# Performance work log

Hardware: AMD Instinct MI355X
Metric: run time of the kernel (lower is better)

Reference implementation:

```python
import jax, jax.numpy as jnp
import numpy as np

B, S, H, K = 8, 2048, 768, 128
FILTERS = (1, 3, 5)
C = H // len(FILTERS)  # 256 channels per conv, concat -> H
LN_EPS = 1e-05
COS_EPS = 1e-08


def setup_inputs() -> dict:
    key = jax.random.key(0)
    ks = jax.random.split(key, 16)
    mk = lambda k, shape: jax.random.normal(k, shape, dtype=jnp.float32) * 0.02
    return {
        "representation": jax.random.normal(ks[0], (B, S, H), dtype=jnp.float32),
        "src_mask": jnp.ones((B, S), dtype=jnp.float32),
        # conv weights stored as [k, H_in, C_out] for lax 1D conv (torch Conv2d(1,C,(k,H)))
        "enc_conv_w1": mk(ks[1], (1, H, C)),
        "enc_conv_w3": mk(ks[2], (3, H, C)),
        "enc_conv_w5": mk(ks[3], (5, H, C)),
        "ln_g": jnp.ones((H,), jnp.float32),
        "ln_b": jnp.zeros((H,), jnp.float32),
        "enc_lin_w": mk(ks[4], (H, H)),   # torch Linear weight [out,in]
        "enc_tr_w": mk(ks[5], (K, H)),
        "dec_tr_w": mk(ks[6], (H, K)),
        "dec_conv_w1": mk(ks[7], (1, H, C)),
        "dec_conv_w3": mk(ks[8], (3, H, C)),
        "dec_conv_w5": mk(ks[9], (5, H, C)),
        "dec_lin_w": mk(ks[10], (H, H)),
        "out_lin_w": mk(ks[11], (H, H)),
    }


def _multi_conv(x, ws):
    # x: [B, S, H]; each w: [k, H, C]; torch pads (k//2, 0) -> same-length for odd k
    outs = []
    for w in ws:
        k = w.shape[0]
        outs.append(jax.lax.conv_general_dilated(
            x, w, window_strides=(1,), padding=[(k // 2, k // 2)],
            dimension_numbers=("NWC", "WIO", "NWC")))
    return jnp.concatenate(outs, axis=-1)  # [B, S, H]


def _layernorm(x, g, b):
    mu = jnp.mean(x, axis=-1, keepdims=True)
    var = jnp.mean((x - mu) ** 2, axis=-1, keepdims=True)
    return (x - mu) * jax.lax.rsqrt(var + LN_EPS) * g + b


def reference(representation, src_mask, enc_conv_w1, enc_conv_w3, enc_conv_w5,
              ln_g, ln_b, enc_lin_w, enc_tr_w, dec_tr_w,
              dec_conv_w1, dec_conv_w3, dec_conv_w5, dec_lin_w, out_lin_w):
    # ---- AutoEncoder (dropout layers are identity in eval mode) ----
    h = _multi_conv(representation, (enc_conv_w1, enc_conv_w3, enc_conv_w5))
    h = _layernorm(h + representation, ln_g, ln_b)
    h = jnp.tanh(h @ enc_lin_w.T)
    location = h @ enc_tr_w.T            # [B, S, K] (encode_out)
    d = location @ dec_tr_w.T            # [B, S, H]
    d = _multi_conv(d, (dec_conv_w1, dec_conv_w3, dec_conv_w5))
    d = jnp.tanh(d @ dec_lin_w.T)
    decode_out = d @ out_lin_w.T         # [B, S, H]

    # ---- banded pairwise cosine similarity (fuses the torch shift loop) ----
    # torch loop writes dis_matrix[b, i, i+s+1] = cos(loc[b, i+s+1], loc[b, i])
    # for s in range(max_act_len), i.e. the strict upper band of the symmetric
    # pairwise cosine-similarity matrix with offsets 1..max_act_len.
    normed = location / jnp.maximum(
        jnp.sqrt(jnp.sum(location * location, axis=-1, keepdims=True)), COS_EPS)
    sim = jnp.einsum("bid,bjd->bij", normed, normed)  # [B, S, S]
    offs = jnp.arange(S)[None, :] - jnp.arange(S)[:, None]  # j - i
    max_act_len = jnp.max(jnp.sum(src_mask, axis=-1)).astype(jnp.int32)
    band = (offs >= 1) & (offs <= max_act_len)        # [S, S]
    dis_matrix = jnp.where(band[None], sim, 0.0)
    src_dis_mask = src_mask[:, :, None] * src_mask[:, None, :]
    act_dis_tags = band[None].astype(jnp.float32) * src_dis_mask
    return (location, dis_matrix, act_dis_tags, decode_out)
```

## Files before the change

kernel.cpp:

```cpp
#include <hip/hip_runtime.h>

#define B_   8
#define S_   2048
#define H_   768
#define K_   128
#define C_   256
#define SH_  2052
#define MTOK (B_*S_)

typedef __attribute__((ext_vector_type(8))) short short8;
typedef __attribute__((ext_vector_type(4))) float f32x4;

typedef __attribute__((address_space(1))) const void gvoid;
typedef __attribute__((address_space(3))) void lvoid;

__device__ __forceinline__ void gload16(const void* g, void* l) {
    __builtin_amdgcn_global_load_lds((gvoid*)g, (lvoid*)l, 16, 0, 0);
}

__device__ __forceinline__ ushort f2b(float f) {
    union { float f; unsigned u; } v; v.f = f;
    unsigned r = v.u + 0x7fffu + ((v.u >> 16) & 1u);
    return (ushort)(r >> 16);
}
__device__ __forceinline__ float b2f(ushort u) {
    union { unsigned u; float f; } v; v.u = ((unsigned)u) << 16;
    return v.f;
}
__device__ __forceinline__ float fast_tanh(float x) {
    float e = __expf(2.f * x);
    return 1.f - 2.f / (e + 1.f);
}


__global__ __launch_bounds__(512) void k_maxlen(const float* __restrict__ mask, int* Lp,
                                                ushort* __restrict__ lh) {
    __shared__ float sh[8];
    const int tid = threadIdx.x;
    float mx = 0.f;
    for (int b = 0; b < B_; ++b) {
        const float4 v = ((const float4*)(mask + b * S_))[tid];
        float s = v.x + v.y + v.z + v.w;
#pragma unroll
        for (int off = 32; off; off >>= 1) s += __shfl_xor(s, off);
        if ((tid & 63) == 0) sh[tid >> 6] = s;
        __syncthreads();
        if (tid == 0) {
            float t = 0.f;
#pragma unroll
            for (int q = 0; q < 8; ++q) t += sh[q];
            mx = fmaxf(mx, t);
        }
        __syncthreads();
    }
    if (tid == 0) *Lp = (int)mx;
    for (int i = tid; i < B_ * 4 * K_; i += 512) {
        const int b = i >> 9;
        const int rc = i & 511;
        const int rr = rc >> 7;
        const int cc = rc & 127;
        const int row = (rr < 2) ? rr : (2048 + rr);
        lh[((size_t)b * SH_ + row) * K_ + cc] = 0;
    }
}

__global__ void k_build_xh(const float* __restrict__ rep, ushort* __restrict__ xh) {
    int i = blockIdx.x * blockDim.x + threadIdx.x;
    const int stride = gridDim.x * blockDim.x;
    const int n4 = B_ * SH_ * H_ / 4;
    for (; i < n4; i += stride) {
        const int idx = i * 4;
        const int h = idx % H_;
        const int rs = idx / H_;
        const int s = rs % SH_;
        const int b = rs / SH_;
        ushort4 o; o.x = 0; o.y = 0; o.z = 0; o.w = 0;
        if (s >= 2 && s < S_ + 2) {
            const float4 v = *(const float4*)(rep + ((size_t)b * S_ + (s - 2)) * H_ + h);
            o.x = f2b(v.x); o.y = f2b(v.y); o.z = f2b(v.z); o.w = f2b(v.w);
        }
        *(ushort4*)(xh + idx) = o;
    }
}

struct CvtE { const float* src; ushort* dst; int n; int kh; int sld; };
struct CvtAll { CvtE e[11]; };

__global__ void k_cvt_all(CvtAll a) {
    const CvtE e = a.e[blockIdx.y];
    int i = blockIdx.x * blockDim.x + threadIdx.x;
    const int stride = gridDim.x * blockDim.x;
    for (; i < e.n; i += stride) {
        if (e.kh) {
            const int c = i / e.kh;
            const int r = i - c * e.kh;
            e.dst[i] = f2b(e.src[r * e.sld + c]);
        } else {
            e.dst[i] = f2b(e.src[i]);
        }
    }
}


struct CompE { const ushort* w; int wld; int woff; ushort* o; int old_; int koff; };
struct CompP { const ushort* dtrT; CompE e[9]; };

__global__ __launch_bounds__(256) void k_compw(CompP p) {
    __shared__ __align__(16) ushort As[128 * 64];
    __shared__ __align__(16) ushort Bs[128 * 64];
    const CompE e = p.e[blockIdx.y];
    const int tid = threadIdx.x;
    const int w = tid >> 6, lane = tid & 63;
    const int l15 = lane & 15, lk = lane >> 4;
    const int wr = w >> 1, wc = w & 1;
    const int n_base = blockIdx.x * 128;
    f32x4 acc[4][4] = {};
    const int srow = lane >> 3;
    const int scol = (lane & 7) * 8;

    for (int kt = 0; kt < 12; ++kt) {
        const int kk = kt << 6;
#pragma unroll
        for (int q = 0; q < 4; ++q) {
            const int r = w * 32 + q * 8;
            gload16(p.dtrT + (size_t)(r + srow) * 768 + kk + scol, As + r * 64);
            gload16(e.w + (size_t)(n_base + r + srow) * e.wld + e.woff + kk + scol, Bs + r * 64);
        }
        __syncthreads();
#pragma unroll
        for (int ks = 0; ks < 2; ++ks) {
            short8 af[4], bfr[4];
#pragma unroll
            for (int i = 0; i < 4; ++i)
                af[i] = *(const short8*)(As + (wr * 64 + i * 16 + l15) * 64 + ks * 32 + 8 * lk);
#pragma unroll
            for (int j = 0; j < 4; ++j)
                bfr[j] = *(const short8*)(Bs + (wc * 64 + j * 16 + l15) * 64 + ks * 32 + 8 * lk);
#pragma unroll
            for (int i = 0; i < 4; ++i)
#pragma unroll
                for (int j = 0; j < 4; ++j)
                    acc[i][j] = __builtin_amdgcn_mfma_f32_16x16x32_bf16(af[i], bfr[j], acc[i][j], 0, 0, 0);
        }
        __syncthreads();
    }
#pragma unroll
    for (int i = 0; i < 4; ++i)
#pragma unroll
        for (int j = 0; j < 4; ++j)
#pragma unroll
            for (int jj = 0; jj < 4; ++jj) {
                const int jr = wr * 64 + i * 16 + 4 * lk + jj;
                const int c  = n_base + wc * 64 + j * 16 + l15;
                e.o[(size_t)c * e.old_ + e.koff + jr] = f2b(acc[i][j][jj]);
            }
}


struct G3P {
    const ushort* A;
    const ushort* W0;
    const ushort* W1;
    const ushort* W2;
    int lda;
    ushort* outB; int ldoB;
    int nMtiles;
};

template<bool DEC>
__global__ __launch_bounds__(512, 2) void g3(G3P p) {
    constexpr int TPT = DEC ? 2 : 12;
    constexpr int LDA = DEC ? 128 : 768;
    constexpr int ASEG = 1024;
    constexpr int BSEG = 2048;
    constexpr int BUFE = (ASEG + BSEG) * 8;
    __shared__ __align__(16) ushort lds[3][BUFE];

    const int tid = threadIdx.x;
    const int w = tid >> 6, lane = tid & 63;
    const int l15 = lane & 15, lk = lane >> 4;
    const int wr = w >> 2, wc = w & 3;
    const int axor = l15 & 7;

    const int nM = p.nMtiles;
    int idx = blockIdx.x;
    int br;
    if (idx < nM) br = 2;
    else if (idx < 2 * nM) { br = 1; idx -= nM; }
    else { br = 0; idx -= 2 * nM; }
    const int m_base = idx * 128;
    const int n_base = br * 256;
    const int nt = TPT * (2 * br + 1);
    const int Ktot = LDA * (2 * br + 1);
    const ushort* Wt = (br == 0) ? p.W0 : (br == 1) ? p.W1 : p.W2;
    const int arow0 = m_base + ((m_base >> 11) << 2) + (2 - br);

    auto stage1 = [&](int kt, int bufi, int q) {
        const int tap = kt / TPT;
        const int h0 = (kt - tap * TPT) << 6;
        if (q < 2) {
            const int seg = q * 512 + tid;
            const int row = seg >> 3;
            const int slot = (seg & 7) ^ (row & 7);
            gload16(p.A + (size_t)(arow0 + tap + row) * LDA + h0 + slot * 8,
                    &lds[bufi][seg * 8]);
        } else {
            const int seg = (q - 2) * 512 + tid;
            const int row = seg >> 3;
            const int slot = (seg & 7) ^ (row & 7);
            gload16(Wt + (size_t)row * Ktot + (kt << 6) + slot * 8,
                    &lds[bufi][ASEG * 8 + seg * 8]);
        }
    };
    auto stage = [&](int kt, int bufi) {
#pragma unroll
        for (int q = 0; q < 6; ++q) stage1(kt, bufi, q);
    };

    f32x4 acc[4][4] = {};

    stage(0, 0);
    stage(1, 1);

    int buf = 0;
    for (int t = 0; t < nt; ++t) {
        const ushort* Ab = &lds[buf][0];
        const ushort* Bb = &lds[buf][ASEG * 8];
        if (t + 1 < nt) asm volatile("s_waitcnt vmcnt(6)" ::: "memory");
        else            asm volatile("s_waitcnt vmcnt(0)" ::: "memory");
        __builtin_amdgcn_sched_barrier(0);
        asm volatile("s_barrier" ::: "memory");
        __builtin_amdgcn_sched_barrier(0);

        int nbuf = buf + 2; if (nbuf >= 3) nbuf -= 3;
        const bool sb = (t + 2 < nt);

#pragma unroll
        for (int ks = 0; ks < 2; ++ks) {
            short8 bq[4], aq[4];
#pragma unroll
            for (int ni = 0; ni < 4; ++ni)
                bq[ni] = *(const short8*)(Bb + (wc * 64 + ni * 16 + l15) * 64 + ((((ks << 2) | lk) ^ axor) << 3));
#pragma unroll
            for (int mi = 0; mi < 4; ++mi)
                aq[mi] = *(const short8*)(Ab + (wr * 64 + mi * 16 + l15) * 64 + ((((ks << 2) | lk) ^ axor) << 3));
            if (sb) { stage1(t + 2, nbuf, 3 * ks); stage1(t + 2, nbuf, 3 * ks + 1); stage1(t + 2, nbuf, 3 * ks + 2); }
            asm volatile("s_waitcnt lgkmcnt(0)" ::: "memory");
            __builtin_amdgcn_sched_barrier(0);
            __builtin_amdgcn_s_setprio(1);
#pragma unroll
            for (int mi = 0; mi < 4; ++mi)
#pragma unroll
                for (int ni = 0; ni < 4; ++ni)
                    acc[mi][ni] = __builtin_amdgcn_mfma_f32_16x16x32_bf16(aq[mi], bq[ni], acc[mi][ni], 0, 0, 0);
            __builtin_amdgcn_s_setprio(0);
            __builtin_amdgcn_sched_barrier(0);
        }
        ++buf; if (buf == 3) buf = 0;
    }

#pragma unroll
    for (int mi = 0; mi < 4; ++mi)
#pragma unroll
        for (int ni = 0; ni < 4; ++ni)
#pragma unroll
            for (int jj = 0; jj < 4; ++jj) {
                const int r = m_base + wr * 64 + mi * 16 + 4 * lk + jj;
                const int n = n_base + wc * 64 + ni * 16 + l15;
                p.outB[(size_t)r * p.ldoB + n] = f2b(acc[mi][ni][jj]);
            }
}


struct G4P {
    const ushort* A;
    const ushort* W;
    int Ktot;
    int lda;
    ushort* outB; int ldoB;
    float*  outF; int ldoF;
    int act;
};

__global__ __launch_bounds__(256, 2) void g4(G4P p) {
    constexpr int ASEG = 1024;
    constexpr int BSEG = 1536;
    __shared__ __align__(16) ushort lds[2][(ASEG + BSEG) * 8];

    const int tid = threadIdx.x;
    const int w = tid >> 6, lane = tid & 63;
    const int l15 = lane & 15, lk = lane >> 4;
    const int wr = w >> 1, wc = w & 1;
    const int axor = l15 & 7;
    const int m_base = blockIdx.x * 128;
    const int n_base = blockIdx.y * 192;
    const int nt = p.Ktot >> 6;

    auto stage = [&](int kt, int bufi) {
        const int kk = kt << 6;
        ushort* Ab = &lds[bufi][0];
        ushort* Bb = &lds[bufi][ASEG * 8];
#pragma unroll
        for (int q = 0; q < 4; ++q) {
            const int seg = q * 256 + tid;
            const int row = seg >> 3;
            const int s = (seg & 7) ^ (row & 7);
            gload16(p.A + (size_t)(m_base + row) * p.lda + kk + s * 8, Ab + seg * 8);
        }
#pragma unroll
        for (int q = 0; q < 6; ++q) {
            const int seg = q * 256 + tid;
            const int row = seg >> 3;
            const int s = (seg & 7) ^ (row & 7);
            gload16(p.W + (size_t)(n_base + row) * p.Ktot + kk + s * 8, Bb + seg * 8);
        }
    };

    f32x4 acc[4][6] = {};

    stage(0, 0);
    stage(1, 1);

    for (int t = 0; t < nt; ++t) {
        const int cur = t & 1;
        const ushort* Ab = &lds[cur][0];
        const ushort* Bb = &lds[cur][ASEG * 8];
        if (t + 1 < nt) asm volatile("s_waitcnt vmcnt(10)" ::: "memory");
        else            asm volatile("s_waitcnt vmcnt(0)" ::: "memory");
        __builtin_amdgcn_sched_barrier(0);
        asm volatile("s_barrier" ::: "memory");
        __builtin_amdgcn_sched_barrier(0);

        short8 af[4][2], bf[6][2];
#pragma unroll
        for (int mi = 0; mi < 4; ++mi)
#pragma unroll
            for (int ks = 0; ks < 2; ++ks)
                af[mi][ks] = *(const short8*)(Ab + (wr * 64 + mi * 16 + l15) * 64 + ((((ks << 2) | lk) ^ axor) << 3));
#pragma unroll
        for (int ni = 0; ni < 6; ++ni)
#pragma unroll
            for (int ks = 0; ks < 2; ++ks)
                bf[ni][ks] = *(const short8*)(Bb + (wc * 96 + ni * 16 + l15) * 64 + ((((ks << 2) | lk) ^ axor) << 3));
        asm volatile("s_waitcnt lgkmcnt(0)" ::: "memory");
        __builtin_amdgcn_sched_barrier(0);
        asm volatile("s_barrier" ::: "memory");
        __builtin_amdgcn_sched_barrier(0);
        if (t + 2 < nt) stage(t + 2, cur);
        __builtin_amdgcn_sched_barrier(0);
        __builtin_amdgcn_s_setprio(1);
#pragma unroll
        for (int mi = 0; mi < 4; ++mi)
#pragma unroll
            for (int ni = 0; ni < 6; ++ni) {
                acc[mi][ni] = __builtin_amdgcn_mfma_f32_16x16x32_bf16(af[mi][0], bf[ni][0], acc[mi][ni], 0, 0, 0);
                acc[mi][ni] = __builtin_amdgcn_mfma_f32_16x16x32_bf16(af[mi][1], bf[ni][1], acc[mi][ni], 0, 0, 0);
            }
        __builtin_amdgcn_s_setprio(0);
        __builtin_amdgcn_sched_barrier(0);
    }

#pragma unroll
    for (int mi = 0; mi < 4; ++mi)
#pragma unroll
        for (int ni = 0; ni < 6; ++ni)
#pragma unroll
            for (int jj = 0; jj < 4; ++jj) {
                const int r = m_base + wr * 64 + mi * 16 + 4 * lk + jj;
                const int n = n_base + wc * 96 + ni * 16 + l15;
                float v = acc[mi][ni][jj];
                if (p.act) v = fast_tanh(v);
                if (p.outF) p.outF[(size_t)r * p.ldoF + n] = v;
                if (p.outB) p.outB[(size_t)r * p.ldoB + n] = f2b(v);
            }
}


struct GemmP {
    const ushort* A;
    const ushort* Wt;
    int Ktot;
    int lda;
    ushort* outB;
    int ldoB;
    int outB_halo;
    float* outF;
    int ldoF;
    int act;
};

template<int BM, int BN>
__global__ __launch_bounds__(256) void gemm_lds(GemmP p) {
    constexpr int MF = BM / 32;
    constexpr int NF = BN / 32;
    __shared__ __align__(16) ushort As[BM * 64];
    __shared__ __align__(16) ushort Bs[BN * 64];
    const int tid = threadIdx.x;
    const int w = tid >> 6, lane = tid & 63;
    const int l15 = lane & 15, lk = lane >> 4;
    const int m_base = blockIdx.x * BM;
    const int n_base = blockIdx.y * BN;
    const int wr = w >> 1, wc = w & 1;
    f32x4 acc[MF][NF] = {};
    const int srow = lane >> 3;
    const int scol = (lane & 7) * 8;
    const int nk = p.Ktot >> 6;

    for (int kt = 0; kt < nk; ++kt) {
        const int kk = kt << 6;
#pragma unroll
        for (int q = 0; q < BM / 32; ++q) {
            const int r = w * (BM / 4) + q * 8;
            gload16(p.A + (size_t)(m_base + r + srow) * p.lda + kk + scol, As + r * 64);
        }
#pragma unroll
        for (int q = 0; q < BN / 32; ++q) {
            const int r = w * (BN / 4) + q * 8;
            gload16(p.Wt + (size_t)(n_base + r + srow) * p.Ktot + kk + scol, Bs + r * 64);
        }
        __syncthreads();
#pragma unroll
        for (int ks = 0; ks < 2; ++ks) {
            short8 af[MF], bfr[NF];
#pragma unroll
            for (int i = 0; i < MF; ++i)
                af[i] = *(const short8*)(As + (wr * (BM / 2) + i * 16 + l15) * 64 + ks * 32 + 8 * lk);
#pragma unroll
            for (int j = 0; j < NF; ++j)
                bfr[j] = *(const short8*)(Bs + (wc * (BN / 2) + j * 16 + l15) * 64 + ks * 32 + 8 * lk);
#pragma unroll
            for (int i = 0; i < MF; ++i)
#pragma unroll
                for (int j = 0; j < NF; ++j)
                    acc[i][j] = __builtin_amdgcn_mfma_f32_16x16x32_bf16(af[i], bfr[j], acc[i][j], 0, 0, 0);
        }
        __syncthreads();
    }

    const int bb4 = ((m_base >> 11) << 2) + 2;
#pragma unroll
    for (int i = 0; i < MF; ++i)
#pragma unroll
        for (int j = 0; j < NF; ++j)
#pragma unroll
            for (int jj = 0; jj < 4; ++jj) {
                const int r = m_base + wr * (BM / 2) + i * 16 + 4 * lk + jj;
                const int n = n_base + wc * (BN / 2) + j * 16 + l15;
                float v = acc[i][j][jj];
                if (p.act) v = fast_tanh(v);
                if (p.outF) p.outF[(size_t)r * p.ldoF + n] = v;
                if (p.outB) {
                    const int rr = p.outB_halo ? (r + bb4) : r;
                    p.outB[(size_t)rr * p.ldoB + n] = f2b(v);
                }
            }
}


__global__ __launch_bounds__(192) void k_ln(const ushort* __restrict__ conv,
                                            const float* __restrict__ rep,
                                            const float* __restrict__ gw,
                                            const float* __restrict__ bw,
                                            ushort* __restrict__ out) {
    const int row = blockIdx.x;
    const int tid = threadIdx.x;
    const int h = tid * 4;
    const ushort4 cv = *(const ushort4*)(conv + (size_t)row * H_ + h);
    const float4  rv = *(const float4*)(rep + (size_t)row * H_ + h);
    float v[4] = { b2f(cv.x) + rv.x, b2f(cv.y) + rv.y, b2f(cv.z) + rv.z, b2f(cv.w) + rv.w };
    float s1 = v[0] + v[1] + v[2] + v[3];
    float s2 = v[0]*v[0] + v[1]*v[1] + v[2]*v[2] + v[3]*v[3];
#pragma unroll
    for (int off = 32; off; off >>= 1) { s1 += __shfl_xor(s1, off); s2 += __shfl_xor(s2, off); }
    __shared__ float sh[6];
    const int wid = tid >> 6, lane = tid & 63;
    if (lane == 0) { sh[wid] = s1; sh[3 + wid] = s2; }
    __syncthreads();
    s1 = sh[0] + sh[1] + sh[2];
    s2 = sh[3] + sh[4] + sh[5];
    const float mu  = s1 * (1.f / H_);
    const float var = s2 * (1.f / H_) - mu * mu;
    const float rs  = rsqrtf(var + 1e-5f);
    const float4 gv = *(const float4*)(gw + h);
    const float4 bv = *(const float4*)(bw + h);
    ushort4 o;
    o.x = f2b((v[0] - mu) * rs * gv.x + bv.x);
    o.y = f2b((v[1] - mu) * rs * gv.y + bv.y);
    o.z = f2b((v[2] - mu) * rs * gv.z + bv.z);
    o.w = f2b((v[3] - mu) * rs * gv.w + bv.w);
    *(ushort4*)(out + (size_t)row * H_ + h) = o;
}


__global__ __launch_bounds__(256) void k_normed(const float* __restrict__ loc, ushort* __restrict__ out) {
    const int wid = threadIdx.x >> 6, lane = threadIdx.x & 63;
    const int row = blockIdx.x * 4 + wid;
    const float* lp = loc + (size_t)row * K_;
    const float x0 = lp[lane], x1 = lp[lane + 64];
    float ss = x0 * x0 + x1 * x1;
#pragma unroll
    for (int off = 32; off; off >>= 1) ss += __shfl_xor(ss, off);
    const float sc = 1.f / fmaxf(sqrtf(ss), 1e-8f);
    ushort* op = out + (size_t)row * K_;
    op[lane] = f2b(x0 * sc);
    op[lane + 64] = f2b(x1 * sc);
}


__global__ __launch_bounds__(256) void k_simtags(const ushort* __restrict__ normed,
                                                 const float* __restrict__ mask,
                                                 const int* __restrict__ Lp,
                                                 float* __restrict__ dis,
                                                 float* __restrict__ tags) {
    const int wid = threadIdx.x >> 6, lane = threadIdx.x & 63;
    const int l15 = lane & 15, lk = lane >> 4;
    const int b   = blockIdx.z;
    const int i0b = blockIdx.x * 64;
    const int i0  = i0b + wid * 16;
    const int j0  = blockIdx.y * 64;
    const int L   = *Lp;
    f32x4 acc[4] = {};
    if ((j0 + 63 >= i0b + 1) && (j0 <= i0b + 63 + L)) {
        const ushort* nb = normed + (size_t)b * S_ * K_;
#pragma unroll
        for (int kt = 0; kt < 4; ++kt) {
            const int kk = kt * 32;
            const short8 a = *(const short8*)(nb + (size_t)(i0 + l15) * K_ + kk + 8 * lk);
#pragma unroll
            for (int j = 0; j < 4; ++j) {
                const short8 bfr = *(const short8*)(nb + (size_t)(j0 + j * 16 + l15) * K_ + kk + 8 * lk);
                acc[j] = __builtin_amdgcn_mfma_f32_16x16x32_bf16(a, bfr, acc[j], 0, 0, 0);
            }
        }
    }
    const float* mb = mask + b * S_;
    float* dp = dis  + (size_t)b * S_ * S_;
    float* tp = tags + (size_t)b * S_ * S_;
#pragma unroll
    for (int j = 0; j < 4; ++j) {
#pragma unroll
        for (int jj = 0; jj < 4; ++jj) {
            const int i  = i0 + 4 * lk + jj;
            const int jc = j0 + j * 16 + l15;
            const int d  = jc - i;
            const bool band = (d >= 1 && d <= L);
            dp[(size_t)i * S_ + jc] = band ? acc[j][jj] : 0.f;
            tp[(size_t)i * S_ + jc] = band ? mb[i] * mb[jc] : 0.f;
        }
    }
}


extern "C" void kernel_launch(void* const* d_in, const int* in_sizes, int n_in,
                              void* d_out, int out_size, void* d_ws, size_t ws_size,
                              hipStream_t stream) {
    const float* rep  = (const float*)d_in[0];
    const float* mask = (const float*)d_in[1];
    const float* ew1  = (const float*)d_in[2];
    const float* ew3  = (const float*)d_in[3];
    const float* ew5  = (const float*)d_in[4];
    const float* lng  = (const float*)d_in[5];
    const float* lnb  = (const float*)d_in[6];
    const float* elin = (const float*)d_in[7];
    const float* etr  = (const float*)d_in[8];
    const float* dtr  = (const float*)d_in[9];
    const float* dw1  = (const float*)d_in[10];
    const float* dw3  = (const float*)d_in[11];
    const float* dw5  = (const float*)d_in[12];
    const float* dlin = (const float*)d_in[13];
    const float* olin = (const float*)d_in[14];

    float* out_loc = (float*)d_out;
    float* out_dis = out_loc + (size_t)B_ * S_ * K_;
    float* out_tag = out_dis + (size_t)B_ * S_ * S_;
    float* out_dec = out_tag + (size_t)B_ * S_ * S_;

    char* ws = (char*)d_ws;
    size_t off = 0;
    auto alloc = [&](size_t bytes) -> char* {
        char* p = ws + off;
        off += (bytes + 255) & ~(size_t)255;
        return p;
    };
    int*    Lp    = (int*)alloc(256);
    ushort* Xh    = (ushort*)alloc((size_t)B_ * SH_ * H_ * 2);
    ushort* bufLh = (ushort*)alloc((size_t)B_ * SH_ * K_ * 2);
    ushort* wte1  = (ushort*)alloc((size_t)C_ * 768 * 2);
    ushort* wte3  = (ushort*)alloc((size_t)C_ * 2304 * 2);
    ushort* wte5  = (ushort*)alloc((size_t)C_ * 3840 * 2);
    ushort* wtd1  = (ushort*)alloc((size_t)C_ * 768 * 2);
    ushort* wtd3  = (ushort*)alloc((size_t)C_ * 2304 * 2);
    ushort* wtd5  = (ushort*)alloc((size_t)C_ * 3840 * 2);
    ushort* welin = (ushort*)alloc((size_t)H_ * H_ * 2);
    ushort* wetr  = (ushort*)alloc((size_t)K_ * H_ * 2);
    ushort* dtrT  = (ushort*)alloc((size_t)K_ * H_ * 2);
    ushort* wdlin = (ushort*)alloc((size_t)H_ * H_ * 2);
    ushort* wolin = (ushort*)alloc((size_t)H_ * H_ * 2);
    ushort* wc1   = (ushort*)alloc((size_t)C_ * 128 * 2);
    ushort* wc3   = (ushort*)alloc((size_t)C_ * 384 * 2);
    ushort* wc5   = (ushort*)alloc((size_t)C_ * 640 * 2);
    ushort* bufB  = (ushort*)alloc((size_t)MTOK * H_ * 2);
    ushort* bufC  = (ushort*)alloc((size_t)MTOK * H_ * 2);
    ushort* bufD  = (ushort*)alloc((size_t)MTOK * H_ * 2);
    ushort* bufN  = (ushort*)alloc((size_t)MTOK * K_ * 2);
    if (ws_size < off) return;

    k_maxlen<<<1, 512, 0, stream>>>(mask, Lp, bufLh);
    k_build_xh<<<2048, 256, 0, stream>>>(rep, Xh);

    CvtAll ca;
    ca.e[0]  = { ew1,  wte1, 768 * C_,  768,  C_ };
    ca.e[1]  = { ew3,  wte3, 2304 * C_, 2304, C_ };
    ca.e[2]  = { ew5,  wte5, 3840 * C_, 3840, C_ };
    ca.e[3]  = { dw1,  wtd1, 768 * C_,  768,  C_ };
    ca.e[4]  = { dw3,  wtd3, 2304 * C_, 2304, C_ };
    ca.e[5]  = { dw5,  wtd5, 3840 * C_, 3840, C_ };
    ca.e[6]  = { elin, welin, H_ * H_, 0, 0 };
    ca.e[7]  = { etr,  wetr,  K_ * H_, 0, 0 };
    ca.e[8]  = { dlin, wdlin, H_ * H_, 0, 0 };
    ca.e[9]  = { olin, wolin, H_ * H_, 0, 0 };
    ca.e[10] = { dtr,  dtrT,  K_ * H_, 768, K_ };
    k_cvt_all<<<dim3(256, 11), 256, 0, stream>>>(ca);

    {
        CompP cp; cp.dtrT = dtrT;
        cp.e[0] = { wtd1, 768,  0,        wc1, 128, 0 };
        for (int t = 0; t < 3; ++t) cp.e[1 + t] = { wtd3, 2304, t * 768, wc3, 384, t * 128 };
        for (int t = 0; t < 5; ++t) cp.e[4 + t] = { wtd5, 3840, t * 768, wc5, 640, t * 128 };
        k_compw<<<dim3(2, 9), 256, 0, stream>>>(cp);
    }

    {
        G3P p{}; p.A = Xh; p.W0 = wte1; p.W1 = wte3; p.W2 = wte5;
        p.lda = H_; p.outB = bufB; p.ldoB = H_; p.nMtiles = MTOK / 128;
        g3<false><<<3 * (MTOK / 128), 512, 0, stream>>>(p);
    }
    k_ln<<<MTOK, 192, 0, stream>>>(bufB, rep, lng, lnb, bufC);
    {
        G4P p{}; p.A = bufC; p.W = welin; p.Ktot = H_; p.lda = H_;
        p.outB = bufD; p.ldoB = H_; p.act = 1;
        g4<<<dim3(MTOK / 128, H_ / 192), 256, 0, stream>>>(p);
    }
    {
        GemmP p{}; p.A = bufD; p.lda = H_; p.Wt = wetr; p.Ktot = H_;
        p.outF = out_loc; p.ldoF = K_; p.outB = bufLh; p.ldoB = K_; p.outB_halo = 1;
        gemm_lds<64, 128><<<dim3(MTOK / 64, 1), 256, 0, stream>>>(p);
    }
    k_normed<<<MTOK / 4, 256, 0, stream>>>(out_loc, bufN);
    {
        G3P p{}; p.A = bufLh; p.W0 = wc1; p.W1 = wc3; p.W2 = wc5;
        p.lda = K_; p.outB = bufB; p.ldoB = H_; p.nMtiles = MTOK / 128;
        g3<true><<<3 * (MTOK / 128), 512, 0, stream>>>(p);
    }
    {
        G4P p{}; p.A = bufB; p.W = wdlin; p.Ktot = H_; p.lda = H_;
        p.outB = bufC; p.ldoB = H_; p.act = 1;
        g4<<<dim3(MTOK / 128, H_ / 192), 256, 0, stream>>>(p);
    }
    {
        G4P p{}; p.A = bufC; p.W = wolin; p.Ktot = H_; p.lda = H_;
        p.outF = out_dec; p.ldoF = H_;
        g4<<<dim3(MTOK / 128, H_ / 192), 256, 0, stream>>>(p);
    }
    k_simtags<<<dim3(S_ / 64, S_ / 64, B_), 256, 0, stream>>>(bufN, mask, Lp, out_dis, out_tag);
}
```

Measured before the change: 386.9 us.

## Retile conv GEMM to 128x128 double-buffer, fuse residual add and cosine normalization

The multi-tap conv GEMM changes from 512-thread 128x256 tiles with a 3-stage LDS ring to 256-thread 128x128 tiles with double buffering. Each step now loads all fragments up front, then issues the next prefetch after a second barrier. The residual add of the input representation moves from the layernorm kernel into the encoder conv epilogue. The location GEMM now computes row norms in its epilogue and writes the normalized bf16 copy directly, which removes the separate k_normed kernel and its reread of location. In exchange the residual is added before bf16 rounding, which changes numerics slightly, and the smaller tiles give less reuse per block.

```diff
diff --git a/kernel.cpp b/kernel.cpp
--- a/kernel.cpp
+++ b/kernel.cpp
@@ -157,64 +157,62 @@
 }
 
 
-struct G3P {
+struct G5P {
     const ushort* A;
     const ushort* W0;
     const ushort* W1;
     const ushort* W2;
-    int lda;
+    const float* rep;
     ushort* outB; int ldoB;
-    int nMtiles;
 };
 
 template<bool DEC>
-__global__ __launch_bounds__(512, 2) void g3(G3P p) {
+__global__ __launch_bounds__(256, 2) void g5(G5P p) {
     constexpr int TPT = DEC ? 2 : 12;
     constexpr int LDA = DEC ? 128 : 768;
     constexpr int ASEG = 1024;
-    constexpr int BSEG = 2048;
-    constexpr int BUFE = (ASEG + BSEG) * 8;
-    __shared__ __align__(16) ushort lds[3][BUFE];
+    constexpr int BSEG = 1024;
+    __shared__ __align__(16) ushort lds[2][(ASEG + BSEG) * 8];
 
     const int tid = threadIdx.x;
     const int w = tid >> 6, lane = tid & 63;
     const int l15 = lane & 15, lk = lane >> 4;
-    const int wr = w >> 2, wc = w & 3;
+    const int wr = w >> 1, wc = w & 1;
     const int axor = l15 & 7;
 
-    const int nM = p.nMtiles;
     int idx = blockIdx.x;
     int br;
-    if (idx < nM) br = 2;
-    else if (idx < 2 * nM) { br = 1; idx -= nM; }
-    else { br = 0; idx -= 2 * nM; }
-    const int m_base = idx * 128;
-    const int n_base = br * 256;
+    if (idx < 256) br = 2;
+    else if (idx < 512) { br = 1; idx -= 256; }
+    else { br = 0; idx -= 512; }
+    const int m_base = (idx & 127) * 128;
+    const int nb_loc = idx >> 7;
+    const int n_base = br * 256 + nb_loc * 128;
     const int nt = TPT * (2 * br + 1);
     const int Ktot = LDA * (2 * br + 1);
-    const ushort* Wt = (br == 0) ? p.W0 : (br == 1) ? p.W1 : p.W2;
-    const int arow0 = m_base + ((m_base >> 11) << 2) + (2 - br);
-
-    auto stage1 = [&](int kt, int bufi, int q) {
+    const ushort* Wt = ((br == 0) ? p.W0 : (br == 1) ? p.W1 : p.W2) + (size_t)nb_loc * 128 * Ktot;
+    const int bb = m_base >> 11;
+    const int arow0 = m_base + 4 * bb + (2 - br);
+
+    auto stage = [&](int kt, int bufi) {
         const int tap = kt / TPT;
         const int h0 = (kt - tap * TPT) << 6;
-        if (q < 2) {
-            const int seg = q * 512 + tid;
+        ushort* Ab = &lds[bufi][0];
+        ushort* Bb = &lds[bufi][ASEG * 8];
+#pragma unroll
+        for (int q = 0; q < 4; ++q) {
+            const int seg = q * 256 + tid;
             const int row = seg >> 3;
-            const int slot = (seg & 7) ^ (row & 7);
-            gload16(p.A + (size_t)(arow0 + tap + row) * LDA + h0 + slot * 8,
-                    &lds[bufi][seg * 8]);
-        } else {
-            const int seg = (q - 2) * 512 + tid;
+            const int s = (seg & 7) ^ (row & 7);
+            gload16(p.A + (size_t)(arow0 + tap + row) * LDA + h0 + s * 8, Ab + seg * 8);
+        }
+#pragma unroll
+        for (int q = 0; q < 4; ++q) {
+            const int seg = q * 256 + tid;
             const int row = seg >> 3;
-            const int slot = (seg & 7) ^ (row & 7);
-            gload16(Wt + (size_t)row * Ktot + (kt << 6) + slot * 8,
-                    &lds[bufi][ASEG * 8 + seg * 8]);
-        }
-    };
-    auto stage = [&](int kt, int bufi) {
-#pragma unroll
-        for (int q = 0; q < 6; ++q) stage1(kt, bufi, q);
+            const int s = (seg & 7) ^ (row & 7);
+            gload16(Wt + (size_t)row * Ktot + (kt << 6) + s * 8, Bb + seg * 8);
+        }
     };
 
     f32x4 acc[4][4] = {};
@@ -222,41 +220,43 @@
     stage(0, 0);
     stage(1, 1);
 
-    int buf = 0;
     for (int t = 0; t < nt; ++t) {
-        const ushort* Ab = &lds[buf][0];
-        const ushort* Bb = &lds[buf][ASEG * 8];
-        if (t + 1 < nt) asm volatile("s_waitcnt vmcnt(6)" ::: "memory");
+        const int cur = t & 1;
+        const ushort* Ab = &lds[cur][0];
+        const ushort* Bb = &lds[cur][ASEG * 8];
+        if (t + 1 < nt) asm volatile("s_waitcnt vmcnt(8)" ::: "memory");
         else            asm volatile("s_waitcnt vmcnt(0)" ::: "memory");
         __builtin_amdgcn_sched_barrier(0);
         asm volatile("s_barrier" ::: "memory");
         __builtin_amdgcn_sched_barrier(0);
 
-        int nbuf = buf + 2; if (nbuf >= 3) nbuf -= 3;
-        const bool sb = (t + 2 < nt);
-
-#pragma unroll
-        for (int ks = 0; ks < 2; ++ks) {
-            short8 bq[4], aq[4];
-#pragma unroll
-            for (int ni = 0; ni < 4; ++ni)
-                bq[ni] = *(const short8*)(Bb + (wc * 64 + ni * 16 + l15) * 64 + ((((ks << 2) | lk) ^ axor) << 3));
-#pragma unroll
-            for (int mi = 0; mi < 4; ++mi)
-                aq[mi] = *(const short8*)(Ab + (wr * 64 + mi * 16 + l15) * 64 + ((((ks << 2) | lk) ^ axor) << 3));
-            if (sb) { stage1(t + 2, nbuf, 3 * ks); stage1(t + 2, nbuf, 3 * ks + 1); stage1(t + 2, nbuf, 3 * ks + 2); }
-            asm volatile("s_waitcnt lgkmcnt(0)" ::: "memory");
-            __builtin_amdgcn_sched_barrier(0);
-            __builtin_amdgcn_s_setprio(1);
-#pragma unroll
-            for (int mi = 0; mi < 4; ++mi)
-#pragma unroll
-                for (int ni = 0; ni < 4; ++ni)
-                    acc[mi][ni] = __builtin_amdgcn_mfma_f32_16x16x32_bf16(aq[mi], bq[ni], acc[mi][ni], 0, 0, 0);
-            __builtin_amdgcn_s_setprio(0);
-            __builtin_amdgcn_sched_barrier(0);
-        }
-        ++buf; if (buf == 3) buf = 0;
+        short8 af[4][2], bf[4][2];
+#pragma unroll
+        for (int mi = 0; mi < 4; ++mi)
+#pragma unroll
+            for (int ks = 0; ks < 2; ++ks)
+                af[mi][ks] = *(const short8*)(Ab + (wr * 64 + mi * 16 + l15) * 64 + ((((ks << 2) | lk) ^ axor) << 3));
+#pragma unroll
+        for (int ni = 0; ni < 4; ++ni)
+#pragma unroll
+            for (int ks = 0; ks < 2; ++ks)
+                bf[ni][ks] = *(const short8*)(Bb + (wc * 64 + ni * 16 + l15) * 64 + ((((ks << 2) | lk) ^ axor) << 3));
+        asm volatile("s_waitcnt lgkmcnt(0)" ::: "memory");
+        __builtin_amdgcn_sched_barrier(0);
+        asm volatile("s_barrier" ::: "memory");
+        __builtin_amdgcn_sched_barrier(0);
+        if (t + 2 < nt) stage(t + 2, cur);
+        __builtin_amdgcn_sched_barrier(0);
+        __builtin_amdgcn_s_setprio(1);
+#pragma unroll
+        for (int mi = 0; mi < 4; ++mi)
+#pragma unroll
+            for (int ni = 0; ni < 4; ++ni) {
+                acc[mi][ni] = __builtin_amdgcn_mfma_f32_16x16x32_bf16(af[mi][0], bf[ni][0], acc[mi][ni], 0, 0, 0);
+                acc[mi][ni] = __builtin_amdgcn_mfma_f32_16x16x32_bf16(af[mi][1], bf[ni][1], acc[mi][ni], 0, 0, 0);
+            }
+        __builtin_amdgcn_s_setprio(0);
+        __builtin_amdgcn_sched_barrier(0);
     }
 
 #pragma unroll
@@ -267,7 +267,9 @@
             for (int jj = 0; jj < 4; ++jj) {
                 const int r = m_base + wr * 64 + mi * 16 + 4 * lk + jj;
                 const int n = n_base + wc * 64 + ni * 16 + l15;
-                p.outB[(size_t)r * p.ldoB + n] = f2b(acc[mi][ni][jj]);
+                float v = acc[mi][ni][jj];
+                if (!DEC && p.rep) v += p.rep[(size_t)r * H_ + n];
+                p.outB[(size_t)r * p.ldoB + n] = f2b(v);
             }
 }
 
@@ -376,89 +378,91 @@
 }
 
 
-struct GemmP {
+struct GLP {
     const ushort* A;
     const ushort* Wt;
-    int Ktot;
-    int lda;
-    ushort* outB;
-    int ldoB;
-    int outB_halo;
     float* outF;
-    int ldoF;
-    int act;
+    ushort* outH;
+    ushort* outN;
 };
 
-template<int BM, int BN>
-__global__ __launch_bounds__(256) void gemm_lds(GemmP p) {
-    constexpr int MF = BM / 32;
-    constexpr int NF = BN / 32;
-    __shared__ __align__(16) ushort As[BM * 64];
-    __shared__ __align__(16) ushort Bs[BN * 64];
+__global__ __launch_bounds__(256) void gemm_loc(GLP p) {
+    __shared__ __align__(16) ushort As[64 * 64];
+    __shared__ __align__(16) ushort Bs[128 * 64];
+    __shared__ float rowss[64][2];
     const int tid = threadIdx.x;
     const int w = tid >> 6, lane = tid & 63;
     const int l15 = lane & 15, lk = lane >> 4;
-    const int m_base = blockIdx.x * BM;
-    const int n_base = blockIdx.y * BN;
+    const int m_base = blockIdx.x * 64;
     const int wr = w >> 1, wc = w & 1;
-    f32x4 acc[MF][NF] = {};
+    f32x4 acc[2][4] = {};
     const int srow = lane >> 3;
     const int scol = (lane & 7) * 8;
-    const int nk = p.Ktot >> 6;
-
-    for (int kt = 0; kt < nk; ++kt) {
+
+    for (int kt = 0; kt < 12; ++kt) {
         const int kk = kt << 6;
 #pragma unroll
-        for (int q = 0; q < BM / 32; ++q) {
-            const int r = w * (BM / 4) + q * 8;
-            gload16(p.A + (size_t)(m_base + r + srow) * p.lda + kk + scol, As + r * 64);
-        }
-#pragma unroll
-        for (int q = 0; q < BN / 32; ++q) {
-            const int r = w * (BN / 4) + q * 8;
-            gload16(p.Wt + (size_t)(n_base + r + srow) * p.Ktot + kk + scol, Bs + r * 64);
+        for (int q = 0; q < 2; ++q) {
+            const int r = w * 16 + q * 8;
+            gload16(p.A + (size_t)(m_base + r + srow) * H_ + kk + scol, As + r * 64);
+        }
+#pragma unroll
+        for (int q = 0; q < 4; ++q) {
+            const int r = w * 32 + q * 8;
+            gload16(p.Wt + (size_t)(r + srow) * H_ + kk + scol, Bs + r * 64);
         }
         __syncthreads();
 #pragma unroll
         for (int ks = 0; ks < 2; ++ks) {
-            short8 af[MF], bfr[NF];
-#pragma unroll
-            for (int i = 0; i < MF; ++i)
-                af[i] = *(const short8*)(As + (wr * (BM / 2) + i * 16 + l15) * 64 + ks * 32 + 8 * lk);
-#pragma unroll
-            for (int j = 0; j < NF; ++j)
-                bfr[j] = *(const short8*)(Bs + (wc * (BN / 2) + j * 16 + l15) * 64 + ks * 32 + 8 * lk);
-#pragma unroll
-            for (int i = 0; i < MF; ++i)
-#pragma unroll
-                for (int j = 0; j < NF; ++j)
+            short8 af[2], bfr[4];
+#pragma unroll
+            for (int i = 0; i < 2; ++i)
+                af[i] = *(const short8*)(As + (wr * 32 + i * 16 + l15) * 64 + ks * 32 + 8 * lk);
+#pragma unroll
+            for (int j = 0; j < 4; ++j)
+                bfr[j] = *(const short8*)(Bs + (wc * 64 + j * 16 + l15) * 64 + ks * 32 + 8 * lk);
+#pragma unroll
+            for (int i = 0; i < 2; ++i)
+#pragma unroll
+                for (int j = 0; j < 4; ++j)
                     acc[i][j] = __builtin_amdgcn_mfma_f32_16x16x32_bf16(af[i], bfr[j], acc[i][j], 0, 0, 0);
         }
         __syncthreads();
     }
 
+#pragma unroll
+    for (int i = 0; i < 2; ++i)
+#pragma unroll
+        for (int jj = 0; jj < 4; ++jj) {
+            float s = acc[i][0][jj] * acc[i][0][jj] + acc[i][1][jj] * acc[i][1][jj]
+                    + acc[i][2][jj] * acc[i][2][jj] + acc[i][3][jj] * acc[i][3][jj];
+#pragma unroll
+            for (int off = 1; off < 16; off <<= 1) s += __shfl_xor(s, off);
+            if (l15 == 0) rowss[wr * 32 + i * 16 + 4 * lk + jj][wc] = s;
+        }
+    __syncthreads();
+
     const int bb4 = ((m_base >> 11) << 2) + 2;
 #pragma unroll
-    for (int i = 0; i < MF; ++i)
-#pragma unroll
-        for (int j = 0; j < NF; ++j)
+    for (int i = 0; i < 2; ++i)
+#pragma unroll
+        for (int j = 0; j < 4; ++j)
 #pragma unroll
             for (int jj = 0; jj < 4; ++jj) {
-                const int r = m_base + wr * (BM / 2) + i * 16 + 4 * lk + jj;
-                const int n = n_base + wc * (BN / 2) + j * 16 + l15;
-                float v = acc[i][j][jj];
-                if (p.act) v = fast_tanh(v);
-                if (p.outF) p.outF[(size_t)r * p.ldoF + n] = v;
-                if (p.outB) {
-                    const int rr = p.outB_halo ? (r + bb4) : r;
-                    p.outB[(size_t)rr * p.ldoB + n] = f2b(v);
-                }
+                const int lr = wr * 32 + i * 16 + 4 * lk + jj;
+                const int r  = m_base + lr;
+                const int n  = wc * 64 + j * 16 + l15;
+                const float v = acc[i][j][jj];
+                const float ss = rowss[lr][0] + rowss[lr][1];
+                const float sc = 1.f / fmaxf(sqrtf(ss), 1e-8f);
+                p.outF[(size_t)r * K_ + n] = v;
+                p.outH[(size_t)(r + bb4) * K_ + n] = f2b(v);
+                p.outN[(size_t)r * K_ + n] = f2b(v * sc);
             }
 }
 
 
 __global__ __launch_bounds__(192) void k_ln(const ushort* __restrict__ conv,
-                                            const float* __restrict__ rep,
                                             const float* __restrict__ gw,
                                             const float* __restrict__ bw,
                                             ushort* __restrict__ out) {
@@ -466,8 +470,7 @@
     const int tid = threadIdx.x;
     const int h = tid * 4;
     const ushort4 cv = *(const ushort4*)(conv + (size_t)row * H_ + h);
-    const float4  rv = *(const float4*)(rep + (size_t)row * H_ + h);
-    float v[4] = { b2f(cv.x) + rv.x, b2f(cv.y) + rv.y, b2f(cv.z) + rv.z, b2f(cv.w) + rv.w };
+    float v[4] = { b2f(cv.x), b2f(cv.y), b2f(cv.z), b2f(cv.w) };
     float s1 = v[0] + v[1] + v[2] + v[3];
     float s2 = v[0]*v[0] + v[1]*v[1] + v[2]*v[2] + v[3]*v[3];
 #pragma unroll
@@ -489,21 +492,6 @@
     o.z = f2b((v[2] - mu) * rs * gv.z + bv.z);
     o.w = f2b((v[3] - mu) * rs * gv.w + bv.w);
     *(ushort4*)(out + (size_t)row * H_ + h) = o;
-}
-
-
-__global__ __launch_bounds__(256) void k_normed(const float* __restrict__ loc, ushort* __restrict__ out) {
-    const int wid = threadIdx.x >> 6, lane = threadIdx.x & 63;
-    const int row = blockIdx.x * 4 + wid;
-    const float* lp = loc + (size_t)row * K_;
-    const float x0 = lp[lane], x1 = lp[lane + 64];
-    float ss = x0 * x0 + x1 * x1;
-#pragma unroll
-    for (int off = 32; off; off >>= 1) ss += __shfl_xor(ss, off);
-    const float sc = 1.f / fmaxf(sqrtf(ss), 1e-8f);
-    ushort* op = out + (size_t)row * K_;
-    op[lane] = f2b(x0 * sc);
-    op[lane + 64] = f2b(x1 * sc);
 }
 
 
@@ -631,26 +619,24 @@
     }
 
     {
-        G3P p{}; p.A = Xh; p.W0 = wte1; p.W1 = wte3; p.W2 = wte5;
-        p.lda = H_; p.outB = bufB; p.ldoB = H_; p.nMtiles = MTOK / 128;
-        g3<false><<<3 * (MTOK / 128), 512, 0, stream>>>(p);
-    }
-    k_ln<<<MTOK, 192, 0, stream>>>(bufB, rep, lng, lnb, bufC);
+        G5P p{}; p.A = Xh; p.W0 = wte1; p.W1 = wte3; p.W2 = wte5;
+        p.rep = rep; p.outB = bufB; p.ldoB = H_;
+        g5<false><<<768, 256, 0, stream>>>(p);
+    }
+    k_ln<<<MTOK, 192, 0, stream>>>(bufB, lng, lnb, bufC);
     {
         G4P p{}; p.A = bufC; p.W = welin; p.Ktot = H_; p.lda = H_;
         p.outB = bufD; p.ldoB = H_; p.act = 1;
         g4<<<dim3(MTOK / 128, H_ / 192), 256, 0, stream>>>(p);
     }
     {
-        GemmP p{}; p.A = bufD; p.lda = H_; p.Wt = wetr; p.Ktot = H_;
-        p.outF = out_loc; p.ldoF = K_; p.outB = bufLh; p.ldoB = K_; p.outB_halo = 1;
-        gemm_lds<64, 128><<<dim3(MTOK / 64, 1), 256, 0, stream>>>(p);
-    }
-    k_normed<<<MTOK / 4, 256, 0, stream>>>(out_loc, bufN);
+        GLP p{ bufD, wetr, out_loc, bufLh, bufN };
+        gemm_loc<<<MTOK / 64, 256, 0, stream>>>(p);
+    }
     {
-        G3P p{}; p.A = bufLh; p.W0 = wc1; p.W1 = wc3; p.W2 = wc5;
-        p.lda = K_; p.outB = bufB; p.ldoB = H_; p.nMtiles = MTOK / 128;
-        g3<true><<<3 * (MTOK / 128), 512, 0, stream>>>(p);
+        G5P p{}; p.A = bufLh; p.W0 = wc1; p.W1 = wc3; p.W2 = wc5;
+        p.rep = nullptr; p.outB = bufB; p.ldoB = H_;
+        g5<true><<<768, 256, 0, stream>>>(p);
     }
     {
         G4P p{}; p.A = bufB; p.W = wdlin; p.Ktot = H_; p.lda = H_;
```

Measured after the change: 410.3 us. 6.0% more time.
